# Performance work log

Measured on AMD Instinct MI355X. Metric: run time of the kernel, lower is better.

## Reference

```python
import jax, jax.numpy as jnp
import numpy as np

LMAX, MMAX = 4, 2
K = (LMAX + 1) ** 2                                 # 25 SH coefficients (l-major node layout)
NL = [LMAX - m + 1 for m in range(MMAX + 1)]        # coeffs per order m: [5,4,3]
M_COEFF = NL[0] + sum(2 * n for n in NL[1:])        # 19 coeffs in m-major (mmax-truncated) edge layout
SPHERE_C, HIDDEN_C = 64, 64
NUM_HEADS, ALPHA_C, VALUE_C, OUT_C = 8, 32, 16, 64
P_GRID = 100
N_NODES, N_EDGES = 4096, 24576
NUM_SPECIES, EDGE_C, EMB_C = 90, 64, 64
N_EXTRA = NUM_HEADS * ALPHA_C + HIDDEN_C            # extra m=0 channels for S2_SEP: alpha + gate scalars


def _ln(x, g, b, eps=1e-5):
    mu = jnp.mean(x, -1, keepdims=True)
    var = jnp.var(x, -1, keepdims=True)
    return (x - mu) * jax.lax.rsqrt(var + eps) * g + b


def _smooth_leaky_relu(x, neg=0.2):
    return 0.5 * (1.0 + neg) * x + 0.5 * (1.0 - neg) * x * (2.0 * jax.nn.sigmoid(x) - 1.0)


def _segment_softmax(a, seg, n):
    amax = jax.lax.stop_gradient(jax.ops.segment_max(a, seg, num_segments=n))
    amax = jnp.where(jnp.isfinite(amax), amax, 0.0)
    e = jnp.exp(a - amax[seg])
    s = jax.ops.segment_sum(e, seg, num_segments=n)
    return e / (s[seg] + 1e-16)


def _so2_conv(x, w0, b0, wms, c_in, c_out, x_edge=None, n_extra=0):
    # x: [E, M_COEFF, c_in] in m-major layout (m=0 block, then per m: real rows then imag rows)
    E = x.shape[0]
    L0 = NL[0]
    x0 = x[:, :L0, :].reshape(E, L0 * c_in)
    if x_edge is not None:
        x0 = x0 * x_edge[:, :L0 * c_in]
    y0 = x0 @ w0 + b0
    extra = None
    if n_extra:
        extra = y0[:, L0 * c_out:]
        y0 = y0[:, :L0 * c_out]
    outs = [y0.reshape(E, L0, c_out)]
    off, rad = L0, L0 * c_in
    for m in range(1, MMAX + 1):
        nl = NL[m]
        xr = x[:, off:off + nl, :]
        xi = x[:, off + nl:off + 2 * nl, :]
        if x_edge is not None:
            s = x_edge[:, rad:rad + nl * c_in].reshape(E, nl, c_in)
            xr, xi = xr * s, xi * s
        xr = xr.reshape(E, nl * c_in)
        xi = xi.reshape(E, nl * c_in)
        half = nl * c_out
        wa, wb = wms[m - 1][:, :half], wms[m - 1][:, half:]
        yr = (xr @ wa - xi @ wb).reshape(E, nl, c_out)  # complex block-matmul
        yi = (xr @ wb + xi @ wa).reshape(E, nl, c_out)
        outs.append(jnp.concatenate([yr, yi], axis=1))
        off += 2 * nl
        rad += nl * c_in
    return jnp.concatenate(outs, axis=1), extra


def setup_inputs():
    key = jax.random.key(0)
    ks = iter(jax.random.split(key, 48))
    def w(shape, fan_in):
        return jax.random.normal(next(ks), shape, jnp.float32) / np.sqrt(fan_in)
    inp = {}
    inp['node_feats'] = jax.random.normal(next(ks), (N_NODES, K, SPHERE_C), jnp.float32)
    inp['node_species'] = jax.random.randint(next(ks), (N_NODES,), 0, NUM_SPECIES)
    inp['edge_distances'] = jax.random.normal(next(ks), (N_EDGES, EDGE_C), jnp.float32)
    inp['senders'] = jax.random.randint(next(ks), (N_EDGES,), 0, N_NODES)
    inp['receivers'] = jax.random.randint(next(ks), (N_EDGES,), 0, N_NODES)
    inp['wigner'] = jax.random.normal(next(ks), (N_EDGES, M_COEFF, K), jnp.float32) / np.sqrt(K)
    inp['snd_emb'] = jax.random.normal(next(ks), (NUM_SPECIES, EMB_C), jnp.float32) * 0.001
    inp['rcv_emb'] = jax.random.normal(next(ks), (NUM_SPECIES, EMB_C), jnp.float32) * 0.001
    ec = EDGE_C + 2 * EMB_C                              # 192 after atom-edge embedding concat
    n_rad = 2 * SPHERE_C * (NL[0] + NL[1] + NL[2])       # 1536 per-edge scales for conv1
    inp['rad_w1'] = w((ec, 64), ec); inp['rad_b1'] = jnp.zeros((64,))
    inp['rad_g1'] = jnp.ones((64,)); inp['rad_be1'] = jnp.zeros((64,))
    inp['rad_w2'] = w((64, 64), 64); inp['rad_b2'] = jnp.zeros((64,))
    inp['rad_g2'] = jnp.ones((64,)); inp['rad_be2'] = jnp.zeros((64,))
    inp['rad_w3'] = w((64, n_rad), 64); inp['rad_b3'] = jnp.ones((n_rad,))
    cin1 = 2 * SPHERE_C
    inp['c1_w0'] = w((NL[0] * cin1, NL[0] * HIDDEN_C + N_EXTRA), NL[0] * cin1)
    inp['c1_b0'] = jnp.zeros((NL[0] * HIDDEN_C + N_EXTRA,))
    inp['c1_wm1'] = w((NL[1] * cin1, 2 * NL[1] * HIDDEN_C), NL[1] * cin1)
    inp['c1_wm2'] = w((NL[2] * cin1, 2 * NL[2] * HIDDEN_C), NL[2] * cin1)
    inp['aln_g'] = jnp.ones((ALPHA_C,)); inp['aln_b'] = jnp.zeros((ALPHA_C,))
    inp['alpha_dot'] = w((NUM_HEADS, ALPHA_C), ALPHA_C)
    inp['to_grid'] = jax.random.normal(next(ks), (P_GRID, M_COEFF), jnp.float32) / np.sqrt(M_COEFF)
    inp['from_grid'] = jax.random.normal(next(ks), (M_COEFF, P_GRID), jnp.float32) / np.sqrt(P_GRID)
    cv = NUM_HEADS * VALUE_C
    inp['c2_w0'] = w((NL[0] * HIDDEN_C, NL[0] * cv), NL[0] * HIDDEN_C)
    inp['c2_b0'] = jnp.zeros((NL[0] * cv,))
    inp['c2_wm1'] = w((NL[1] * HIDDEN_C, 2 * NL[1] * cv), NL[1] * HIDDEN_C)
    inp['c2_wm2'] = w((NL[2] * HIDDEN_C, 2 * NL[2] * cv), NL[2] * HIDDEN_C)
    inp['proj_w'] = w((LMAX + 1, cv, OUT_C), cv)
    inp['proj_b'] = jnp.zeros((OUT_C,))
    return inp


def reference(node_feats, node_species, edge_distances, senders, receivers, wigner,
              snd_emb, rcv_emb, rad_w1, rad_b1, rad_g1, rad_be1, rad_w2, rad_b2,
              rad_g2, rad_be2, rad_w3, rad_b3, c1_w0, c1_b0, c1_wm1, c1_wm2,
              aln_g, aln_b, alpha_dot, to_grid, from_grid,
              c2_w0, c2_b0, c2_wm1, c2_wm2, proj_w, proj_b):
    N = node_feats.shape[0]
    # atom-edge embedding gathers + concat with radial-basis distances
    edge_embeds = jnp.concatenate([edge_distances,
                                   snd_emb[node_species[senders]],
                                   rcv_emb[node_species[receivers]]], axis=1)
    msgs = jnp.concatenate([node_feats[senders], node_feats[receivers]], axis=2)  # [E,25,128]
    msgs = jnp.einsum('emk,ekc->emc', wigner, msgs)                               # rotate to edge frame [E,19,128]
    # radial function -> per-edge input scales for SO2 conv 1
    h = jax.nn.silu(_ln(edge_embeds @ rad_w1 + rad_b1, rad_g1, rad_be1))
    h = jax.nn.silu(_ln(h @ rad_w2 + rad_b2, rad_g2, rad_be2))
    x_edge = h @ rad_w3 + rad_b3
    msgs, x0_extra = _so2_conv(msgs, c1_w0, c1_b0, [c1_wm1, c1_wm2],
                               2 * SPHERE_C, HIDDEN_C, x_edge, N_EXTRA)
    x0_alpha = x0_extra[:, :NUM_HEADS * ALPHA_C]
    x0_gate = x0_extra[:, NUM_HEADS * ALPHA_C:]
    # separable S2 activation: SiLU on sphere grid for l>0, SiLU on scalars for l=0
    grid = jax.nn.silu(jnp.einsum('pm,emc->epc', to_grid, msgs))
    tens = jnp.einsum('mp,epc->emc', from_grid, grid)
    msgs = jnp.concatenate([jax.nn.silu(x0_gate)[:, None, :], tens[:, 1:, :]], axis=1)
    msgs, _ = _so2_conv(msgs, c2_w0, c2_b0, [c2_wm1, c2_wm2], HIDDEN_C, NUM_HEADS * VALUE_C)
    # attention weights: LN -> SmoothLeakyReLU -> dot -> per-receiver softmax
    a = _smooth_leaky_relu(_ln(x0_alpha.reshape(-1, NUM_HEADS, ALPHA_C), aln_g, aln_b))
    alpha = _segment_softmax(jnp.einsum('ehk,hk->eh', a, alpha_dot), receivers, N)
    attn = msgs.reshape(-1, M_COEFF, NUM_HEADS, VALUE_C) * alpha[:, None, :, None]
    msgs = attn.reshape(-1, M_COEFF, NUM_HEADS * VALUE_C)
    msgs = jnp.einsum('emk,emc->ekc', wigner, msgs)    # rotate back (W^T), [E,25,128]
    node = jax.ops.segment_sum(msgs, receivers, num_segments=N)
    # SO3 linear: per-degree-l channel mixing, bias only on l=0
    l_of_k = jnp.asarray(np.repeat(np.arange(LMAX + 1), 2 * np.arange(LMAX + 1) + 1))
    out = jnp.einsum('nkc,kcd->nkd', node, proj_w[l_of_k])
    return out.at[:, 0, :].add(proj_b)
```

## Files before the change

kernel.cpp:

```cpp
#include <hip/hip_runtime.h>

typedef unsigned short u16;
typedef unsigned int u32;
typedef __attribute__((ext_vector_type(8))) short short8;
typedef __attribute__((ext_vector_type(4))) float floatx4;

#define E_EDGES 24576
#define EC 12288
#define N_NODES_C 4096

__device__ __forceinline__ float bf2f(u16 u) {
    union { u32 i; float f; } v; v.i = ((u32)u) << 16; return v.f;
}
__device__ __forceinline__ u16 f2bf(float f) {
    union { float f; u32 i; } v; v.f = f;
    u32 x = v.i;
    u32 r = (x + 0x7fffu + ((x >> 16) & 1u)) >> 16;
    return (u16)r;
}
__device__ __forceinline__ u32 pk_bf16(float a, float b) {
    u32 r;
    asm("v_cvt_pk_bf16_f32 %0, %1, %2" : "=v"(r) : "v"(a), "v"(b));
    return r;
}
__device__ __forceinline__ u32 encf(float f) {
    union { float f; u32 i; } v; v.f = f;
    return (v.i & 0x80000000u) ? ~v.i : (v.i | 0x80000000u);
}
__device__ __forceinline__ float decf(u32 u) {
    union { u32 i; float f; } v;
    v.i = (u & 0x80000000u) ? (u ^ 0x80000000u) : ~u;
    return v.f;
}
__device__ __forceinline__ float sigmoidf_(float x) { return __fdividef(1.f, 1.f + __expf(-x)); }
__device__ __forceinline__ float siluf_(float x) { return x * __fdividef(1.f, 1.f + __expf(-x)); }

__device__ __forceinline__ void gld16(const u16* g, u16* l) {
    __builtin_amdgcn_global_load_lds((const __attribute__((address_space(1))) unsigned int*)g,
                                     (__attribute__((address_space(3))) unsigned int*)l, 16, 0, 0);
}

__global__ void k_diag(float* __restrict__ out, int n) {
    int i = blockIdx.x * 256 + threadIdx.x;
    if (i < n) out[i] = 1000.0f;
}

__global__ void k_transpose(const float* __restrict__ src, u16* __restrict__ dst, int K, int N) {
    int idx = blockIdx.x * 256 + threadIdx.x;
    if (idx >= K * N) return;
    int k = idx / N, n = idx % N;
    dst[n * K + k] = f2bf(src[idx]);
}
__global__ void k_combine(const float* __restrict__ src, u16* __restrict__ dst, int K, int H) {
    int total = 4 * K * H;
    int idx = blockIdx.x * 256 + threadIdx.x;
    if (idx >= total) return;
    int n = idx / (2 * K), k = idx % (2 * K);
    float v;
    if (k < K) v = src[k * 2 * H + n];
    else {
        int kk = k - K;
        if (n < H) v = -src[kk * 2 * H + H + n];
        else       v = src[kk * 2 * H + (n - H)];
    }
    dst[idx] = f2bf(v);
}

__global__ void k_packgrid(const float* __restrict__ tg, const float* __restrict__ fg,
                           u16* __restrict__ tgP, u16* __restrict__ fgP) {
    int idx = blockIdx.x * 256 + threadIdx.x;
    if (idx < 112 * 32) {
        int p = idx >> 5, m = idx & 31;
        tgP[idx] = (p < 100 && m < 19) ? f2bf(tg[p * 19 + m]) : (u16)0;
    }
    int j = idx - 112 * 32;
    if (j >= 0 && j < 32 * 128) {
        int m = j >> 7, k = j & 127;
        fgP[j] = (m < 19 && k < 100) ? f2bf(fg[m * 100 + k]) : (u16)0;
    }
}

__global__ void k_init(u32* __restrict__ nmax, float* __restrict__ nsum, int n) {
    int idx = blockIdx.x * 256 + threadIdx.x;
    if (idx < n) { nmax[idx] = 0x007FFFFFu;  nsum[idx] = 0.f; }
}

__global__ void k_deg(const int* __restrict__ rcv, u32* __restrict__ deg) {
    int e = blockIdx.x * 256 + threadIdx.x;
    if (e < E_EDGES) atomicAdd(&deg[rcv[e]], 1u);
}
__global__ __launch_bounds__(256) void k_pfx(const u32* __restrict__ deg,
                                             u32* __restrict__ rowstart, u32* __restrict__ cur) {
    __shared__ u32 ps[256];
    int t = threadIdx.x;
    u32 loc[16]; u32 s = 0;
#pragma unroll
    for (int i = 0; i < 16; i++) { loc[i] = s; s += deg[t * 16 + i]; }
    ps[t] = s;
    __syncthreads();
    for (int o = 1; o < 256; o <<= 1) {
        u32 v = (t >= o) ? ps[t - o] : 0u;
        __syncthreads();
        ps[t] += v;
        __syncthreads();
    }
    u32 base = (t == 0) ? 0u : ps[t - 1];
#pragma unroll
    for (int i = 0; i < 16; i++) { u32 v = base + loc[i]; rowstart[t * 16 + i] = v; cur[t * 16 + i] = v; }
}
__global__ void k_fill(const int* __restrict__ rcv, u32* __restrict__ cur, int* __restrict__ elist) {
    int e = blockIdx.x * 256 + threadIdx.x;
    if (e < E_EDGES) { u32 p = atomicAdd(&cur[rcv[e]], 1u); elist[p] = e; }
}

__global__ void k_ee(const float* __restrict__ dist, const int* __restrict__ species,
                     const int* __restrict__ snd, const int* __restrict__ rcv,
                     const float* __restrict__ semb, const float* __restrict__ remb,
                     u16* __restrict__ ee) {
    int idx = blockIdx.x * 256 + threadIdx.x;
    if (idx >= E_EDGES * 192) return;
    int e = idx / 192, c = idx % 192;
    float v;
    if (c < 64)       v = dist[e * 64 + c];
    else if (c < 128) v = semb[species[snd[e]] * 64 + (c - 64)];
    else              v = remb[species[rcv[e]] * 64 + (c - 128)];
    ee[idx] = f2bf(v);
}

__global__ __launch_bounds__(256) void k_gemm(
    const u16* __restrict__ A, int lda,
    const u16* __restrict__ BT, int ldb,
    u16* __restrict__ C, int ldc,
    int N, int K,
    const float* __restrict__ bias) {
    __shared__ u16 As[128 * 32];
    __shared__ u16 Bs[128 * 32];
    int tid = threadIdx.x;
    int bm0 = blockIdx.x * 128;
    int bn0 = blockIdx.y * 128;
    int wave = tid >> 6, lane = tid & 63;
    int wm = (wave >> 1) * 64, wn = (wave & 1) * 64;
    int lrow = lane & 15, lk = (lane >> 4) * 8;

    int srow = (wave << 4) + (lane >> 2);
    int schunk = (lane & 3) << 3;
    const u16* Arow0 = A + (size_t)(bm0 + srow) * lda + schunk;
    const u16* Arow1 = A + (size_t)(bm0 + srow + 64) * lda + schunk;
    int n0 = bn0 + srow;      if (n0 >= N) n0 = N - 1;
    int n1 = bn0 + srow + 64; if (n1 >= N) n1 = N - 1;
    const u16* Brow0 = BT + (size_t)n0 * ldb + schunk;
    const u16* Brow1 = BT + (size_t)n1 * ldb + schunk;
    u16* lA0 = &As[srow * 32 + schunk];
    u16* lA1 = &As[(srow + 64) * 32 + schunk];
    u16* lB0 = &Bs[srow * 32 + schunk];
    u16* lB1 = &Bs[(srow + 64) * 32 + schunk];

    floatx4 acc[4][4];
#pragma unroll
    for (int i = 0; i < 4; i++)
#pragma unroll
        for (int j = 0; j < 4; j++) acc[i][j] = floatx4{0.f, 0.f, 0.f, 0.f};

    for (int k0 = 0; k0 < K; k0 += 32) {
        gld16(Arow0 + k0, lA0);
        gld16(Arow1 + k0, lA1);
        gld16(Brow0 + k0, lB0);
        gld16(Brow1 + k0, lB1);
        asm volatile("s_waitcnt vmcnt(0)" ::: "memory");
        __syncthreads();
        short8 a[4], b[4];
#pragma unroll
        for (int i = 0; i < 4; i++) a[i] = *(const short8*)(&As[(wm + i * 16 + lrow) * 32 + lk]);
#pragma unroll
        for (int j = 0; j < 4; j++) b[j] = *(const short8*)(&Bs[(wn + j * 16 + lrow) * 32 + lk]);
#pragma unroll
        for (int i = 0; i < 4; i++)
#pragma unroll
            for (int j = 0; j < 4; j++)
                acc[i][j] = __builtin_amdgcn_mfma_f32_16x16x32_bf16(a[i], b[j], acc[i][j], 0, 0, 0);
        __syncthreads();
    }

    int q = lane >> 4;
#pragma unroll
    for (int i = 0; i < 4; i++) {
#pragma unroll
        for (int j = 0; j < 4; j++) {
            int col = bn0 + wn + j * 16 + lrow;
            if (col < N) {
                float bv = bias ? bias[col] : 0.f;
#pragma unroll
                for (int r = 0; r < 4; r++) {
                    int row = bm0 + wm + i * 16 + q * 4 + r;
                    C[(size_t)row * ldc + col] = f2bf(acc[i][j][r] + bv);
                }
            }
        }
    }
}

__global__ __launch_bounds__(256) void k_ln_silu(const u16* __restrict__ in, u16* __restrict__ out,
                                                 const float* __restrict__ g, const float* __restrict__ b) {
    int tid = threadIdx.x;
    int e = blockIdx.x * 4 + (tid >> 6);
    int c = tid & 63;
    float x = bf2f(in[(size_t)e * 64 + c]);
    float s = x, s2 = x * x;
#pragma unroll
    for (int o = 32; o; o >>= 1) { s += __shfl_xor(s, o); s2 += __shfl_xor(s2, o); }
    float mu = s * (1.f / 64.f);
    float var = s2 * (1.f / 64.f) - mu * mu;
    float rs = rsqrtf(var + 1e-5f);
    float y = (x - mu) * rs * g[c] + b[c];
    out[(size_t)e * 64 + c] = f2bf(siluf_(y));
}

__global__ __launch_bounds__(256) void k_rotate(const float* __restrict__ nf, const float* __restrict__ wig,
                                                const int* __restrict__ snd, const int* __restrict__ rcv,
                                                const u16* __restrict__ xe, u16* __restrict__ A1, int e0) {
    __shared__ float wl[2][475];
    int tid = threadIdx.x;
    for (int i = tid; i < 950; i += 256) {
        int ee = e0 + blockIdx.x * 2 + (i / 475);
        wl[i / 475][i % 475] = wig[(size_t)ee * 475 + (i % 475)];
    }
    __syncthreads();
    int le = tid >> 7, c = tid & 127;
    int el = blockIdx.x * 2 + le;
    int e = e0 + el;
    int nd = (c < 64) ? snd[e] : rcv[e];
    int cc = c & 63;
    float msg[25];
#pragma unroll
    for (int k = 0; k < 25; k++) msg[k] = nf[(size_t)nd * 1600 + k * 64 + cc];
    const float* w = wl[le];
    size_t ebase = (size_t)el * 2432;
    size_t xbase = (size_t)el * 1536;
#pragma unroll
    for (int m = 0; m < 19; m++) {
        float r = 0.f;
#pragma unroll
        for (int k = 0; k < 25; k++) r += w[m * 25 + k] * msg[k];
        int a1c, xc;
        if (m < 5)       { a1c = m * 128;               xc = m * 128; }
        else if (m < 9)  { a1c = 640 + (m - 5) * 128;   xc = 640 + (m - 5) * 128; }
        else if (m < 13) { a1c = 1152 + (m - 9) * 128;  xc = 640 + (m - 9) * 128; }
        else if (m < 16) { a1c = 1664 + (m - 13) * 128; xc = 1152 + (m - 13) * 128; }
        else             { a1c = 2048 + (m - 16) * 128; xc = 1152 + (m - 16) * 128; }
        float sc = bf2f(xe[xbase + xc + c]);
        A1[ebase + a1c + c] = f2bf(r * sc);
    }
}

__global__ __launch_bounds__(256) void k_logits(const u16* __restrict__ Y0, const int* __restrict__ rcv,
                                                const float* __restrict__ g, const float* __restrict__ b,
                                                const float* __restrict__ adot,
                                                float* __restrict__ logits, u32* __restrict__ nmax) {
    int e = blockIdx.x;
    int tid = threadIdx.x;
    int h = tid >> 5, c = tid & 31;
    float x = bf2f(Y0[(size_t)e * 640 + 320 + h * 32 + c]);
    float s = x, s2 = x * x;
#pragma unroll
    for (int o = 16; o; o >>= 1) { s += __shfl_xor(s, o); s2 += __shfl_xor(s2, o); }
    float mu = s * (1.f / 32.f);
    float var = s2 * (1.f / 32.f) - mu * mu;
    float rs = rsqrtf(var + 1e-5f);
    float a = (x - mu) * rs * g[c] + b[c];
    float f = 0.6f * a + 0.4f * a * (2.f * sigmoidf_(a) - 1.f);
    float l = f * adot[h * 32 + c];
#pragma unroll
    for (int o = 16; o; o >>= 1) l += __shfl_xor(l, o);
    if (c == 0) {
        logits[e * 8 + h] = l;
        atomicMax(&nmax[rcv[e] * 8 + h], encf(l));
    }
}

__global__ void k_expsum(const float* __restrict__ logits, const int* __restrict__ rcv,
                         const u32* __restrict__ nmax, float* __restrict__ ealpha, float* __restrict__ nsum) {
    int idx = blockIdx.x * 256 + threadIdx.x;
    if (idx >= E_EDGES * 8) return;
    int e = idx >> 3, h = idx & 7;
    int r = rcv[e];
    float amax = decf(nmax[r * 8 + h]);
    if (!(amax > -1e38f && amax < 1e38f)) amax = 0.f;
    float v = __expf(logits[idx] - amax);
    ealpha[idx] = v;
    atomicAdd(&nsum[r * 8 + h], v);
}

#define GR_XS_STR 40
#define GR_T1_STR 136
__global__ __launch_bounds__(256) void k_grid_mfma(
    const u16* __restrict__ Y0, const u16* __restrict__ Y1, const u16* __restrict__ Y2,
    const u16* __restrict__ tgP, const u16* __restrict__ fgP, u16* __restrict__ A2) {
    __shared__ u16 Xs[128 * GR_XS_STR];
    __shared__ u16 T1s[128 * GR_T1_STR];
    int tid = threadIdx.x;
    int e0 = blockIdx.x * 2;
    {
        int row = tid >> 1;
        uint4 z = {0, 0, 0, 0};
        *(uint4*)(&T1s[row * GR_T1_STR + 112 + (tid & 1) * 8]) = z;
    }
    {
        int mp = tid & 15;
        int c0 = ((tid >> 4) & 7) << 3;
        int le = tid >> 7;
        int e = e0 + le;
        int m0 = 2 * mp, m1 = m0 + 1;
        uint4 va = {0, 0, 0, 0}, vb = {0, 0, 0, 0};
        if (m0 < 5)       va = *(const uint4*)(&Y0[(size_t)e * 640 + m0 * 64 + c0]);
        else if (m0 < 13) va = *(const uint4*)(&Y1[(size_t)e * 512 + (m0 - 5) * 64 + c0]);
        else if (m0 < 19) va = *(const uint4*)(&Y2[(size_t)e * 384 + (m0 - 13) * 64 + c0]);
        if (m1 < 5)       vb = *(const uint4*)(&Y0[(size_t)e * 640 + m1 * 64 + c0]);
        else if (m1 < 13) vb = *(const uint4*)(&Y1[(size_t)e * 512 + (m1 - 5) * 64 + c0]);
        else if (m1 < 19) vb = *(const uint4*)(&Y2[(size_t)e * 384 + (m1 - 13) * 64 + c0]);
        const u16* pa = (const u16*)&va;
        const u16* pb = (const u16*)&vb;
        int rbase = le * 64 + c0;
#pragma unroll
        for (int j = 0; j < 8; j++) {
            u32 w = (u32)pa[j] | ((u32)pb[j] << 16);
            *(u32*)(&Xs[(rbase + j) * GR_XS_STR + 2 * mp]) = w;
        }
    }
    __syncthreads();
    int wave = tid >> 6, lane = tid & 63;
    int wn = wave << 5;
    int ln = lane & 15, q = lane >> 4;
    short8 bx0 = *(const short8*)(&Xs[(wn + ln) * GR_XS_STR + q * 8]);
    short8 bx1 = *(const short8*)(&Xs[(wn + 16 + ln) * GR_XS_STR + q * 8]);
    floatx4 acc1[2][7];
#pragma unroll
    for (int pt = 0; pt < 7; pt++) {
        short8 a = *(const short8*)(&tgP[(size_t)(pt * 16 + ln) * 32 + q * 8]);
        acc1[0][pt] = __builtin_amdgcn_mfma_f32_16x16x32_bf16(a, bx0, floatx4{0.f, 0.f, 0.f, 0.f}, 0, 0, 0);
        acc1[1][pt] = __builtin_amdgcn_mfma_f32_16x16x32_bf16(a, bx1, floatx4{0.f, 0.f, 0.f, 0.f}, 0, 0, 0);
    }
#pragma unroll
    for (int i = 0; i < 2; i++) {
        u16* dst = &T1s[(wn + i * 16 + ln) * GR_T1_STR + q * 4];
#pragma unroll
        for (int pt = 0; pt < 7; pt++) {
            uint2 pv;
            pv.x = pk_bf16(siluf_(acc1[i][pt][0]), siluf_(acc1[i][pt][1]));
            pv.y = pk_bf16(siluf_(acc1[i][pt][2]), siluf_(acc1[i][pt][3]));
            *(uint2*)(dst + pt * 16) = pv;
        }
    }
    __syncthreads();
    floatx4 acc2[2][2];
    acc2[0][0] = floatx4{0.f, 0.f, 0.f, 0.f}; acc2[0][1] = floatx4{0.f, 0.f, 0.f, 0.f};
    acc2[1][0] = floatx4{0.f, 0.f, 0.f, 0.f}; acc2[1][1] = floatx4{0.f, 0.f, 0.f, 0.f};
#pragma unroll
    for (int ks = 0; ks < 4; ks++) {
        short8 c0 = *(const short8*)(&T1s[(wn + ln) * GR_T1_STR + ks * 32 + q * 8]);
        short8 c1 = *(const short8*)(&T1s[(wn + 16 + ln) * GR_T1_STR + ks * 32 + q * 8]);
#pragma unroll
        for (int ct = 0; ct < 2; ct++) {
            short8 b = *(const short8*)(&fgP[(size_t)(ct * 16 + ln) * 128 + ks * 32 + q * 8]);
            acc2[0][ct] = __builtin_amdgcn_mfma_f32_16x16x32_bf16(c0, b, acc2[0][ct], 0, 0, 0);
            acc2[1][ct] = __builtin_amdgcn_mfma_f32_16x16x32_bf16(c1, b, acc2[1][ct], 0, 0, 0);
        }
    }
#pragma unroll
    for (int rt = 0; rt < 2; rt++) {
        int row = wn + rt * 16 + q * 4;
        int e = e0 + (row >> 6), c = row & 63;
#pragma unroll
        for (int ct = 0; ct < 2; ct++) {
            int mp = ct * 16 + ln;
            if (mp >= 1 && mp < 19) {
                uint2 pv;
                pv.x = pk_bf16(acc2[rt][ct][0], acc2[rt][ct][1]);
                pv.y = pk_bf16(acc2[rt][ct][2], acc2[rt][ct][3]);
                *(uint2*)(&A2[(size_t)e * 1216 + mp * 64 + c]) = pv;
            }
        }
    }
    if (tid < 128) {
        int e = e0 + (tid >> 6), c = tid & 63;
        float gate = bf2f(Y0[(size_t)e * 640 + 576 + c]);
        A2[(size_t)e * 1216 + c] = f2bf(siluf_(gate));
    }
}

__global__ __launch_bounds__(128) void k_gather(
    const u16* __restrict__ Z0, const u16* __restrict__ Z1, const u16* __restrict__ Z2,
    const float* __restrict__ wig, const float* __restrict__ ealpha, const float* __restrict__ nsum,
    const u32* __restrict__ rowstart, const u32* __restrict__ deg, const int* __restrict__ elist,
    float* __restrict__ node, int e0, int accum) {
    int n = blockIdx.x;
    int tid = threadIdx.x;
    int h = tid >> 4;
    float acc[25];
#pragma unroll
    for (int k = 0; k < 25; k++) acc[k] = 0.f;
    float sden = __fdividef(1.f, nsum[n * 8 + h] + 1e-16f);
    u32 lo = rowstart[n], hi = lo + deg[n];
    bool did = false;
    for (u32 idx = lo; idx < hi; ++idx) {
        int e = __builtin_amdgcn_readfirstlane(elist[idx]);
        int el = e - e0;
        if ((u32)el >= (u32)EC) continue;
        did = true;
        const float* w = wig + (size_t)e * 475;
        float al = ealpha[e * 8 + h] * sden;
        float s[19];
#pragma unroll
        for (int m = 0; m < 19; m++) {
            float v;
            if (m < 5)       v = bf2f(Z0[(size_t)el * 640 + m * 128 + tid]);
            else if (m < 13) v = bf2f(Z1[(size_t)el * 1024 + (m - 5) * 128 + tid]);
            else             v = bf2f(Z2[(size_t)el * 768 + (m - 13) * 128 + tid]);
            s[m] = v * al;
        }
#pragma unroll
        for (int m = 0; m < 19; m++)
#pragma unroll
            for (int k = 0; k < 25; k++)
                acc[k] = fmaf(w[m * 25 + k], s[m], acc[k]);
    }
    float* nb = node + (size_t)n * 3200 + tid;
    if (accum) {
        if (!did) return;
#pragma unroll
        for (int k = 0; k < 25; k++) nb[k * 128] += acc[k];
    } else {
#pragma unroll
        for (int k = 0; k < 25; k++) nb[k * 128] = acc[k];
    }
}

#define PJ_STR 136
__global__ __launch_bounds__(256) void k_proj_mfma(
    const float* __restrict__ node, const u16* __restrict__ pwTb,
    const float* __restrict__ pb, float* __restrict__ out) {
    __shared__ u16 As[128 * PJ_STR];
    __shared__ u16 Bs[64 * PJ_STR];
    int tid = threadIdx.x;
    int n0 = blockIdx.x * 128;
    int k = blockIdx.y;
    int l = (int)sqrtf((float)k + 0.5f);
#pragma unroll
    for (int it = 0; it < 16; it++) {
        int i = tid + it * 256;
        int row = i >> 5;
        int c0 = (i & 31) << 2;
        float4 v = *(const float4*)(&node[(size_t)(n0 + row) * 3200 + k * 128 + c0]);
        uint2 pv;
        pv.x = pk_bf16(v.x, v.y);
        pv.y = pk_bf16(v.z, v.w);
        *(uint2*)(&As[row * PJ_STR + c0]) = pv;
    }
    const u16* pw = pwTb + (size_t)l * 8192;
#pragma unroll
    for (int jt = 0; jt < 4; jt++) {
        int j = tid + jt * 256;
        int d = j >> 4;
        int c0 = (j & 15) << 3;
        *(uint4*)(&Bs[d * PJ_STR + c0]) = *(const uint4*)(&pw[d * 128 + c0]);
    }
    __syncthreads();
    int wave = tid >> 6, lane = tid & 63;
    int wr = wave * 32;
    int ln = lane & 15, q = lane >> 4;
    floatx4 acc[2][4];
#pragma unroll
    for (int i = 0; i < 2; i++)
#pragma unroll
        for (int j = 0; j < 4; j++) acc[i][j] = floatx4{0.f, 0.f, 0.f, 0.f};
#pragma unroll
    for (int ks = 0; ks < 4; ks++) {
        short8 a0 = *(const short8*)(&As[(wr + ln) * PJ_STR + ks * 32 + q * 8]);
        short8 a1 = *(const short8*)(&As[(wr + 16 + ln) * PJ_STR + ks * 32 + q * 8]);
#pragma unroll
        for (int j = 0; j < 4; j++) {
            short8 b = *(const short8*)(&Bs[(j * 16 + ln) * PJ_STR + ks * 32 + q * 8]);
            acc[0][j] = __builtin_amdgcn_mfma_f32_16x16x32_bf16(a0, b, acc[0][j], 0, 0, 0);
            acc[1][j] = __builtin_amdgcn_mfma_f32_16x16x32_bf16(a1, b, acc[1][j], 0, 0, 0);
        }
    }
#pragma unroll
    for (int rt = 0; rt < 2; rt++)
#pragma unroll
        for (int j = 0; j < 4; j++) {
            int d = j * 16 + ln;
            float bv = (k == 0) ? pb[d] : 0.f;
#pragma unroll
            for (int r = 0; r < 4; r++) {
                int n = n0 + wr + rt * 16 + q * 4 + r;
                out[(size_t)n * 1600 + k * 64 + d] = acc[rt][j][r] + bv;
            }
        }
}

extern "C" void kernel_launch(void* const* d_in, const int* in_sizes, int n_in,
                              void* d_out, int out_size, void* d_ws, size_t ws_size,
                              hipStream_t stream) {
    const float* nf      = (const float*)d_in[0];
    const int* species   = (const int*)d_in[1];
    const float* dist    = (const float*)d_in[2];
    const int* snd       = (const int*)d_in[3];
    const int* rcv       = (const int*)d_in[4];
    const float* wig     = (const float*)d_in[5];
    const float* semb    = (const float*)d_in[6];
    const float* remb    = (const float*)d_in[7];
    const float* rad_w1  = (const float*)d_in[8];
    const float* rad_b1  = (const float*)d_in[9];
    const float* rad_g1  = (const float*)d_in[10];
    const float* rad_be1 = (const float*)d_in[11];
    const float* rad_w2  = (const float*)d_in[12];
    const float* rad_b2  = (const float*)d_in[13];
    const float* rad_g2  = (const float*)d_in[14];
    const float* rad_be2 = (const float*)d_in[15];
    const float* rad_w3  = (const float*)d_in[16];
    const float* rad_b3  = (const float*)d_in[17];
    const float* c1_w0   = (const float*)d_in[18];
    const float* c1_b0   = (const float*)d_in[19];
    const float* c1_wm1  = (const float*)d_in[20];
    const float* c1_wm2  = (const float*)d_in[21];
    const float* aln_g   = (const float*)d_in[22];
    const float* aln_b   = (const float*)d_in[23];
    const float* adot    = (const float*)d_in[24];
    const float* to_grid = (const float*)d_in[25];
    const float* from_grid=(const float*)d_in[26];
    const float* c2_w0   = (const float*)d_in[27];
    const float* c2_b0   = (const float*)d_in[28];
    const float* c2_wm1  = (const float*)d_in[29];
    const float* c2_wm2  = (const float*)d_in[30];
    const float* proj_w  = (const float*)d_in[31];
    const float* proj_b  = (const float*)d_in[32];

    char* ws = (char*)d_ws;
    size_t off = 0;
    auto take = [&](size_t bytes) -> char* {
        char* p = ws + off;
        off += (bytes + 255) & ~(size_t)255;
        return p;
    };
    u16* w_rad1T  = (u16*)take(64 * 192 * 2);
    u16* w_rad2T  = (u16*)take(64 * 64 * 2);
    u16* w_rad3T  = (u16*)take(1536 * 64 * 2);
    u16* w_c1w0T  = (u16*)take(640 * 640 * 2);
    u16* w_c1m1T  = (u16*)take((size_t)512 * 1024 * 2);
    u16* w_c1m2T  = (u16*)take((size_t)384 * 768 * 2);
    u16* w_c2w0T  = (u16*)take((size_t)640 * 320 * 2);
    u16* w_c2m1T  = (u16*)take((size_t)1024 * 512 * 2);
    u16* w_c2m2T  = (u16*)take((size_t)768 * 384 * 2);
    u16* w_tgP    = (u16*)take(112 * 32 * 2);
    u16* w_fgP    = (u16*)take(32 * 128 * 2);
    u16* w_pwT    = (u16*)take(5 * 8192 * 2);
    float* logits = (float*)take((size_t)E_EDGES * 8 * 4);
    float* ealpha = (float*)take((size_t)E_EDGES * 8 * 4);
    u32* nmax     = (u32*)take((size_t)N_NODES_C * 8 * 4);
    float* nsum   = (float*)take((size_t)N_NODES_C * 8 * 4);
    float* node   = (float*)take((size_t)N_NODES_C * 3200 * 4);
    u16* a_h2     = (u16*)take((size_t)E_EDGES * 64 * 2);
    u32* c_deg    = (u32*)take((size_t)N_NODES_C * 4);
    u32* c_row    = (u32*)take((size_t)N_NODES_C * 4);
    u32* c_cur    = (u32*)take((size_t)N_NODES_C * 4);
    int* c_elist  = (int*)take((size_t)E_EDGES * 4);
    char* arena   = take(173015040);
    if (off > ws_size) {
        k_diag<<<(out_size + 255) / 256, 256, 0, stream>>>((float*)d_out, out_size);
        return;
    }

    u16* a_ee   = (u16*)(arena + 0);
    u16* a_ypre = (u16*)(arena + 9437184);
    u16* a_h1   = (u16*)(arena + 12582912);
    u16* a_xe   = (u16*)(arena + 0);
    u16* a_A1   = (u16*)(arena + 37748736);
    u16* a_Y0   = (u16*)(arena + 97517568);
    u16* a_Y1   = (u16*)(arena + 128974848);
    u16* a_Y2   = (u16*)(arena + 154140672);
    u16* a_A2   = (u16*)(arena + 0);
    u16* a_Z0   = (u16*)(arena + 59768832);
    u16* a_Z1   = (u16*)(arena + 75497472);
    u16* a_Z2   = (u16*)(arena + 100663296);

    k_transpose<<<48, 256, 0, stream>>>(rad_w1, w_rad1T, 192, 64);
    k_transpose<<<16, 256, 0, stream>>>(rad_w2, w_rad2T, 64, 64);
    k_transpose<<<384, 256, 0, stream>>>(rad_w3, w_rad3T, 64, 1536);
    k_transpose<<<1600, 256, 0, stream>>>(c1_w0, w_c1w0T, 640, 640);
    k_transpose<<<800, 256, 0, stream>>>(c2_w0, w_c2w0T, 320, 640);
    k_combine<<<2048, 256, 0, stream>>>(c1_wm1, w_c1m1T, 512, 256);
    k_combine<<<1152, 256, 0, stream>>>(c1_wm2, w_c1m2T, 384, 192);
    k_combine<<<2048, 256, 0, stream>>>(c2_wm1, w_c2m1T, 256, 512);
    k_combine<<<1152, 256, 0, stream>>>(c2_wm2, w_c2m2T, 192, 384);
    k_packgrid<<<30, 256, 0, stream>>>(to_grid, from_grid, w_tgP, w_fgP);
    for (int l = 0; l < 5; l++)
        k_transpose<<<32, 256, 0, stream>>>(proj_w + (size_t)l * 8192, w_pwT + (size_t)l * 8192, 128, 64);
    k_init<<<128, 256, 0, stream>>>(nmax, nsum, N_NODES_C * 8);

    hipMemsetAsync(c_deg, 0, (size_t)N_NODES_C * 4, stream);
    k_deg<<<96, 256, 0, stream>>>(rcv, c_deg);
    k_pfx<<<1, 256, 0, stream>>>(c_deg, c_row, c_cur);
    k_fill<<<96, 256, 0, stream>>>(rcv, c_cur, c_elist);

    k_ee<<<(E_EDGES * 192 + 255) / 256, 256, 0, stream>>>(dist, species, snd, rcv, semb, remb, a_ee);
    k_gemm<<<dim3(192, 1), 256, 0, stream>>>(a_ee, 192, w_rad1T, 192, a_ypre, 64, 64, 192, rad_b1);
    k_ln_silu<<<6144, 256, 0, stream>>>(a_ypre, a_h1, rad_g1, rad_be1);
    k_gemm<<<dim3(192, 1), 256, 0, stream>>>(a_h1, 64, w_rad2T, 64, a_ypre, 64, 64, 64, rad_b2);
    k_ln_silu<<<6144, 256, 0, stream>>>(a_ypre, a_h2, rad_g2, rad_be2);

    for (int c = 0; c < 2; c++) {
        int e0 = c * EC;
        k_gemm<<<dim3(96, 12), 256, 0, stream>>>(a_h2 + (size_t)e0 * 64, 64, w_rad3T, 64,
                                                 a_xe, 1536, 1536, 64, rad_b3);
        k_rotate<<<EC / 2, 256, 0, stream>>>(nf, wig, snd, rcv, a_xe, a_A1, e0);
        k_gemm<<<dim3(96, 5), 256, 0, stream>>>(a_A1, 2432, w_c1w0T, 640,
                                                a_Y0 + (size_t)e0 * 640, 640, 640, 640, c1_b0);
        k_gemm<<<dim3(96, 4), 256, 0, stream>>>(a_A1 + 640, 2432, w_c1m1T, 1024,
                                                a_Y1 + (size_t)e0 * 512, 512, 512, 1024, nullptr);
        k_gemm<<<dim3(96, 3), 256, 0, stream>>>(a_A1 + 1664, 2432, w_c1m2T, 768,
                                                a_Y2 + (size_t)e0 * 384, 384, 384, 768, nullptr);
    }

    k_logits<<<E_EDGES, 256, 0, stream>>>(a_Y0, rcv, aln_g, aln_b, adot, logits, nmax);
    k_expsum<<<(E_EDGES * 8 + 255) / 256, 256, 0, stream>>>(logits, rcv, nmax, ealpha, nsum);

    k_grid_mfma<<<E_EDGES / 2, 256, 0, stream>>>(a_Y0, a_Y1, a_Y2, w_tgP, w_fgP, a_A2);

    for (int c = 0; c < 2; c++) {
        int e0 = c * EC;
        k_gemm<<<dim3(96, 5), 256, 0, stream>>>(a_A2 + (size_t)e0 * 1216, 1216, w_c2w0T, 320,
                                                a_Z0, 640, 640, 320, c2_b0);
        k_gemm<<<dim3(96, 8), 256, 0, stream>>>(a_A2 + (size_t)e0 * 1216 + 320, 1216, w_c2m1T, 512,
                                                a_Z1, 1024, 1024, 512, nullptr);
        k_gemm<<<dim3(96, 6), 256, 0, stream>>>(a_A2 + (size_t)e0 * 1216 + 832, 1216, w_c2m2T, 384,
                                                a_Z2, 768, 768, 384, nullptr);
        k_gather<<<N_NODES_C, 128, 0, stream>>>(a_Z0, a_Z1, a_Z2, wig, ealpha, nsum,
                                                c_row, c_deg, c_elist, node, e0, c);
    }

    k_proj_mfma<<<dim3(32, 25), 256, 0, stream>>>(node, w_pwT, proj_b, (float*)d_out);
}
```

Measured before the change: 1.055 ms.

## Stage Wigner tiles in LDS and split gather edges across waves

The gather kernel now loads Wigner matrices for groups of six edges into shared memory, padded for float4 reads, so each weight is fetched from global memory once per block instead of by every thread. The two waves each take alternate edges and each thread handles two heads' channels, then the partial sums are reduced through LDS before the write. Separately, the grid kernel reuses one LDS buffer for both staging arrays, which needs an extra barrier, to shrink shared memory and raise occupancy. The cost is more barriers, doubled accumulator registers and a cross-wave reduction step.

```diff
diff --git a/kernel.cpp b/kernel.cpp
--- a/kernel.cpp
+++ b/kernel.cpp
@@ -295,15 +295,10 @@
 __global__ __launch_bounds__(256) void k_grid_mfma(
     const u16* __restrict__ Y0, const u16* __restrict__ Y1, const u16* __restrict__ Y2,
     const u16* __restrict__ tgP, const u16* __restrict__ fgP, u16* __restrict__ A2) {
-    __shared__ u16 Xs[128 * GR_XS_STR];
     __shared__ u16 T1s[128 * GR_T1_STR];
+    u16* Xs = T1s;
     int tid = threadIdx.x;
     int e0 = blockIdx.x * 2;
-    {
-        int row = tid >> 1;
-        uint4 z = {0, 0, 0, 0};
-        *(uint4*)(&T1s[row * GR_T1_STR + 112 + (tid & 1) * 8]) = z;
-    }
     {
         int mp = tid & 15;
         int c0 = ((tid >> 4) & 7) << 3;
@@ -339,6 +334,12 @@
         acc1[0][pt] = __builtin_amdgcn_mfma_f32_16x16x32_bf16(a, bx0, floatx4{0.f, 0.f, 0.f, 0.f}, 0, 0, 0);
         acc1[1][pt] = __builtin_amdgcn_mfma_f32_16x16x32_bf16(a, bx1, floatx4{0.f, 0.f, 0.f, 0.f}, 0, 0, 0);
     }
+    __syncthreads();
+    {
+        int row = tid >> 1;
+        uint4 z = {0, 0, 0, 0};
+        *(uint4*)(&T1s[row * GR_T1_STR + 112 + (tid & 1) * 8]) = z;
+    }
 #pragma unroll
     for (int i = 0; i < 2; i++) {
         u16* dst = &T1s[(wn + i * 16 + ln) * GR_T1_STR + q * 4];
@@ -387,50 +388,105 @@
     }
 }
 
+#define GT_TS 6
 __global__ __launch_bounds__(128) void k_gather(
     const u16* __restrict__ Z0, const u16* __restrict__ Z1, const u16* __restrict__ Z2,
     const float* __restrict__ wig, const float* __restrict__ ealpha, const float* __restrict__ nsum,
     const u32* __restrict__ rowstart, const u32* __restrict__ deg, const int* __restrict__ elist,
     float* __restrict__ node, int e0, int accum) {
+    __shared__ float wls[GT_TS * 536];
+    __shared__ int es[GT_TS];
+    __shared__ int didAny;
     int n = blockIdx.x;
     int tid = threadIdx.x;
-    int h = tid >> 4;
-    float acc[25];
-#pragma unroll
-    for (int k = 0; k < 25; k++) acc[k] = 0.f;
-    float sden = __fdividef(1.f, nsum[n * 8 + h] + 1e-16f);
-    u32 lo = rowstart[n], hi = lo + deg[n];
-    bool did = false;
-    for (u32 idx = lo; idx < hi; ++idx) {
-        int e = __builtin_amdgcn_readfirstlane(elist[idx]);
-        int el = e - e0;
-        if ((u32)el >= (u32)EC) continue;
-        did = true;
-        const float* w = wig + (size_t)e * 475;
-        float al = ealpha[e * 8 + h] * sden;
-        float s[19];
-#pragma unroll
-        for (int m = 0; m < 19; m++) {
-            float v;
-            if (m < 5)       v = bf2f(Z0[(size_t)el * 640 + m * 128 + tid]);
-            else if (m < 13) v = bf2f(Z1[(size_t)el * 1024 + (m - 5) * 128 + tid]);
-            else             v = bf2f(Z2[(size_t)el * 768 + (m - 13) * 128 + tid]);
-            s[m] = v * al;
-        }
-#pragma unroll
-        for (int m = 0; m < 19; m++)
-#pragma unroll
-            for (int k = 0; k < 25; k++)
-                acc[k] = fmaf(w[m * 25 + k], s[m], acc[k]);
-    }
-    float* nb = node + (size_t)n * 3200 + tid;
-    if (accum) {
-        if (!did) return;
-#pragma unroll
-        for (int k = 0; k < 25; k++) nb[k * 128] += acc[k];
-    } else {
-#pragma unroll
-        for (int k = 0; k < 25; k++) nb[k * 128] = acc[k];
+    int wv = tid >> 6, lane = tid & 63;
+    int h0 = lane >> 4, h1 = 4 + (lane >> 4);
+    float sden0 = __fdividef(1.f, nsum[n * 8 + h0] + 1e-16f);
+    float sden1 = __fdividef(1.f, nsum[n * 8 + h1] + 1e-16f);
+    float acc0[25], acc1[25];
+#pragma unroll
+    for (int k = 0; k < 25; k++) { acc0[k] = 0.f; acc1[k] = 0.f; }
+    if (tid == 0) didAny = 0;
+    u32 lo = rowstart[n], cnt = deg[n];
+    for (u32 base = 0; base < cnt; base += GT_TS) {
+        int nt = (int)((cnt - base) < GT_TS ? (cnt - base) : GT_TS);
+        __syncthreads();
+        if (tid < nt) es[tid] = elist[lo + base + tid];
+        __syncthreads();
+        for (int t = 0; t < nt; t++) {
+            int e = es[t];
+            const float* we = wig + (size_t)e * 475;
+            for (int i = tid; i < 532; i += 128) {
+                int m = i / 28, k = i - m * 28;
+                wls[t * 536 + i] = (k < 25) ? we[m * 25 + k] : 0.f;
+            }
+        }
+        __syncthreads();
+        for (int t = wv; t < nt; t += 2) {
+            int e = es[t];
+            int el = e - e0;
+            if ((u32)el >= (u32)EC) continue;
+            if (lane == 0) didAny = 1;
+            float al0 = ealpha[e * 8 + h0] * sden0;
+            float al1 = ealpha[e * 8 + h1] * sden1;
+            float s0[19], s1[19];
+#pragma unroll
+            for (int m = 0; m < 19; m++) {
+                const u16* zp; int off;
+                if (m < 5)       { zp = Z0; off = el * 640 + m * 128; }
+                else if (m < 13) { zp = Z1; off = el * 1024 + (m - 5) * 128; }
+                else             { zp = Z2; off = el * 768 + (m - 13) * 128; }
+                s0[m] = bf2f(zp[(size_t)off + lane]) * al0;
+                s1[m] = bf2f(zp[(size_t)off + 64 + lane]) * al1;
+            }
+            const float* wt = &wls[t * 536];
+#pragma unroll
+            for (int m = 0; m < 19; m++) {
+#pragma unroll
+                for (int j = 0; j < 6; j++) {
+                    float4 w4 = *(const float4*)(&wt[m * 28 + j * 4]);
+                    acc0[j * 4 + 0] = fmaf(w4.x, s0[m], acc0[j * 4 + 0]);
+                    acc0[j * 4 + 1] = fmaf(w4.y, s0[m], acc0[j * 4 + 1]);
+                    acc0[j * 4 + 2] = fmaf(w4.z, s0[m], acc0[j * 4 + 2]);
+                    acc0[j * 4 + 3] = fmaf(w4.w, s0[m], acc0[j * 4 + 3]);
+                    acc1[j * 4 + 0] = fmaf(w4.x, s1[m], acc1[j * 4 + 0]);
+                    acc1[j * 4 + 1] = fmaf(w4.y, s1[m], acc1[j * 4 + 1]);
+                    acc1[j * 4 + 2] = fmaf(w4.z, s1[m], acc1[j * 4 + 2]);
+                    acc1[j * 4 + 3] = fmaf(w4.w, s1[m], acc1[j * 4 + 3]);
+                }
+                float wl_ = wt[m * 28 + 24];
+                acc0[24] = fmaf(wl_, s0[m], acc0[24]);
+                acc1[24] = fmaf(wl_, s1[m], acc1[24]);
+            }
+        }
+    }
+    __syncthreads();
+    int any = didAny;
+    if (accum && !any) return;
+    float* arr = wls;
+    if (wv == 1) {
+#pragma unroll
+        for (int k = 0; k < 25; k++) {
+            arr[k * 128 + lane] = acc0[k];
+            arr[k * 128 + 64 + lane] = acc1[k];
+        }
+    }
+    __syncthreads();
+    if (wv == 0) {
+        float* nb = node + (size_t)n * 3200;
+        if (accum) {
+#pragma unroll
+            for (int k = 0; k < 25; k++) {
+                nb[k * 128 + lane]      += acc0[k] + arr[k * 128 + lane];
+                nb[k * 128 + 64 + lane] += acc1[k] + arr[k * 128 + 64 + lane];
+            }
+        } else {
+#pragma unroll
+            for (int k = 0; k < 25; k++) {
+                nb[k * 128 + lane]      = acc0[k] + arr[k * 128 + lane];
+                nb[k * 128 + 64 + lane] = acc1[k] + arr[k * 128 + 64 + lane];
+            }
+        }
     }
 }
 
```

New measurement: 1.097 ms. +4.0%, slower.

## Split gather edges across two thread slots and alias grid-kernel LDS buffers

Applied to the files above, without the earlier changes.

The gather kernel now uses 256 threads per node, with two 128-thread slots each handling alternate incoming edges. Their partial sums are combined through shared memory before the single write to the node buffer. This doubles per-node parallelism and memory-level concurrency, at the cost of a block barrier for every pair of edges and an extra LDS reduction. Separately, the grid kernel reuses the T1 shared buffer for the X staging tile, adding a barrier before zeroing its padding. This lowers LDS use per block so more blocks can be resident.

```diff
diff --git a/kernel.cpp b/kernel.cpp
--- a/kernel.cpp
+++ b/kernel.cpp
@@ -295,15 +295,10 @@
 __global__ __launch_bounds__(256) void k_grid_mfma(
     const u16* __restrict__ Y0, const u16* __restrict__ Y1, const u16* __restrict__ Y2,
     const u16* __restrict__ tgP, const u16* __restrict__ fgP, u16* __restrict__ A2) {
-    __shared__ u16 Xs[128 * GR_XS_STR];
     __shared__ u16 T1s[128 * GR_T1_STR];
+    u16* Xs = T1s;
     int tid = threadIdx.x;
     int e0 = blockIdx.x * 2;
-    {
-        int row = tid >> 1;
-        uint4 z = {0, 0, 0, 0};
-        *(uint4*)(&T1s[row * GR_T1_STR + 112 + (tid & 1) * 8]) = z;
-    }
     {
         int mp = tid & 15;
         int c0 = ((tid >> 4) & 7) << 3;
@@ -339,6 +334,12 @@
         acc1[0][pt] = __builtin_amdgcn_mfma_f32_16x16x32_bf16(a, bx0, floatx4{0.f, 0.f, 0.f, 0.f}, 0, 0, 0);
         acc1[1][pt] = __builtin_amdgcn_mfma_f32_16x16x32_bf16(a, bx1, floatx4{0.f, 0.f, 0.f, 0.f}, 0, 0, 0);
     }
+    __syncthreads();
+    {
+        int row = tid >> 1;
+        uint4 z = {0, 0, 0, 0};
+        *(uint4*)(&T1s[row * GR_T1_STR + 112 + (tid & 1) * 8]) = z;
+    }
 #pragma unroll
     for (int i = 0; i < 2; i++) {
         u16* dst = &T1s[(wn + i * 16 + ln) * GR_T1_STR + q * 4];
@@ -387,50 +388,69 @@
     }
 }
 
-__global__ __launch_bounds__(128) void k_gather(
+__global__ __launch_bounds__(256) void k_gather(
     const u16* __restrict__ Z0, const u16* __restrict__ Z1, const u16* __restrict__ Z2,
     const float* __restrict__ wig, const float* __restrict__ ealpha, const float* __restrict__ nsum,
     const u32* __restrict__ rowstart, const u32* __restrict__ deg, const int* __restrict__ elist,
     float* __restrict__ node, int e0, int accum) {
+    __shared__ float mbuf[3200];
+    __shared__ int es_s[2];
+    __shared__ int anyf;
     int n = blockIdx.x;
     int tid = threadIdx.x;
-    int h = tid >> 4;
+    int slot = tid >> 7;
+    int c = tid & 127;
+    int h = c >> 4;
+    if (tid == 0) anyf = 0;
+    float sden = __fdividef(1.f, nsum[n * 8 + h] + 1e-16f);
     float acc[25];
 #pragma unroll
     for (int k = 0; k < 25; k++) acc[k] = 0.f;
-    float sden = __fdividef(1.f, nsum[n * 8 + h] + 1e-16f);
-    u32 lo = rowstart[n], hi = lo + deg[n];
-    bool did = false;
-    for (u32 idx = lo; idx < hi; ++idx) {
-        int e = __builtin_amdgcn_readfirstlane(elist[idx]);
+    u32 lo = rowstart[n], cnt = deg[n];
+    for (u32 base = 0; base < cnt; base += 2) {
+        if (tid < 2) es_s[tid] = (base + tid < cnt) ? elist[lo + base + tid] : -1;
+        __syncthreads();
+        int e = es_s[slot];
         int el = e - e0;
-        if ((u32)el >= (u32)EC) continue;
-        did = true;
-        const float* w = wig + (size_t)e * 475;
-        float al = ealpha[e * 8 + h] * sden;
-        float s[19];
-#pragma unroll
-        for (int m = 0; m < 19; m++) {
-            float v;
-            if (m < 5)       v = bf2f(Z0[(size_t)el * 640 + m * 128 + tid]);
-            else if (m < 13) v = bf2f(Z1[(size_t)el * 1024 + (m - 5) * 128 + tid]);
-            else             v = bf2f(Z2[(size_t)el * 768 + (m - 13) * 128 + tid]);
-            s[m] = v * al;
-        }
-#pragma unroll
-        for (int m = 0; m < 19; m++)
-#pragma unroll
-            for (int k = 0; k < 25; k++)
-                acc[k] = fmaf(w[m * 25 + k], s[m], acc[k]);
-    }
-    float* nb = node + (size_t)n * 3200 + tid;
-    if (accum) {
-        if (!did) return;
-#pragma unroll
-        for (int k = 0; k < 25; k++) nb[k * 128] += acc[k];
-    } else {
-#pragma unroll
-        for (int k = 0; k < 25; k++) nb[k * 128] = acc[k];
+        if (e >= 0 && (u32)el < (u32)EC) {
+            e = __builtin_amdgcn_readfirstlane(e);
+            el = e - e0;
+            if ((tid & 63) == 0) anyf = 1;
+            float al = ealpha[e * 8 + h] * sden;
+            const float* __restrict__ w = wig + (size_t)e * 475;
+            float s[19];
+#pragma unroll
+            for (int m = 0; m < 19; m++) {
+                const u16* zp; int off;
+                if (m < 5)       { zp = Z0; off = el * 640 + m * 128; }
+                else if (m < 13) { zp = Z1; off = el * 1024 + (m - 5) * 128; }
+                else             { zp = Z2; off = el * 768 + (m - 13) * 128; }
+                s[m] = bf2f(zp[(size_t)off + c]) * al;
+            }
+#pragma unroll
+            for (int m = 0; m < 19; m++)
+#pragma unroll
+                for (int k = 0; k < 25; k++)
+                    acc[k] = fmaf(w[m * 25 + k], s[m], acc[k]);
+        }
+        __syncthreads();
+    }
+    if (slot == 1) {
+#pragma unroll
+        for (int k = 0; k < 25; k++) mbuf[k * 128 + c] = acc[k];
+    }
+    __syncthreads();
+    if (slot == 0) {
+        float* nb = node + (size_t)n * 3200 + c;
+        if (accum) {
+            if (anyf) {
+#pragma unroll
+                for (int k = 0; k < 25; k++) nb[k * 128] += acc[k] + mbuf[k * 128 + c];
+            }
+        } else {
+#pragma unroll
+            for (int k = 0; k < 25; k++) nb[k * 128] = acc[k] + mbuf[k * 128 + c];
+        }
     }
 }
 
@@ -633,7 +653,7 @@
                                                 a_Z1, 1024, 1024, 512, nullptr);
         k_gemm<<<dim3(96, 6), 256, 0, stream>>>(a_A2 + (size_t)e0 * 1216 + 832, 1216, w_c2m2T, 384,
                                                 a_Z2, 768, 768, 384, nullptr);
-        k_gather<<<N_NODES_C, 128, 0, stream>>>(a_Z0, a_Z1, a_Z2, wig, ealpha, nsum,
+        k_gather<<<N_NODES_C, 256, 0, stream>>>(a_Z0, a_Z1, a_Z2, wig, ealpha, nsum,
                                                 c_row, c_deg, c_elist, node, e0, c);
     }
 
```

Result: no change. 1.038 ms (-1.6%).
